# Kernel optimization log

Hardware: AMD Instinct MI355X
Metric: run time of the kernel (lower is better)

## Reference

```python
import jax, jax.numpy as jnp
import numpy as np

B, L, C = 4, 2048, 1024
H = 16
D = C // H  # head_dim = 64


def _rope(t, cos, sin):
    # t: [B, H, L, D]; cos/sin: [L, D//2] broadcast to [1, 1, L, D//2]
    te = t[..., ::2]
    to = t[..., 1::2]
    c = cos[None, None]
    s = sin[None, None]
    re = te * c - to * s
    ro = te * s + to * c
    # interleave even/odd back: [..., D//2, 2] -> [..., D]
    return jnp.stack([re, ro], axis=-1).reshape(t.shape)


def setup_inputs() -> dict:
    key = jax.random.key(0)
    ks = jax.random.split(key, 5)
    x = jax.random.normal(ks[0], (B, L, C), dtype=jnp.float32)
    # rotary phases: theta_i = 10000^(-2i/D), angles = pos * theta
    inv_freq = 1.0 / (10000.0 ** (np.arange(0, D, 2, dtype=np.float32) / D))
    ang = np.arange(L, dtype=np.float32)[:, None] * inv_freq[None, :]  # [L, D//2]
    cos = jnp.asarray(np.cos(ang))
    sin = jnp.asarray(np.sin(ang))
    w_qkv = jax.random.normal(ks[1], (3 * C, C), dtype=jnp.float32) * (C ** -0.5)
    w_proj = jax.random.normal(ks[2], (C, C), dtype=jnp.float32) * (C ** -0.5)
    b_proj = jnp.zeros((C,), dtype=jnp.float32)
    return {"x": x, "cos": cos, "sin": sin, "w_qkv": w_qkv, "w_proj": w_proj, "b_proj": b_proj}


def reference(x, cos, sin, w_qkv, w_proj, b_proj):
    Bx, Lx, Cx = x.shape
    # QKV projection (torch Linear: y = x @ W.T), then split heads
    qkv = jnp.einsum("blc,fc->blf", x, w_qkv)  # [B, L, 3C]
    qkv = qkv.reshape(Bx, Lx, 3, H, D).transpose(2, 0, 3, 1, 4)  # [3, B, H, L, D]
    q, k, v = qkv[0], qkv[1], qkv[2]
    q = _rope(q, cos, sin)
    k = _rope(k, cos, sin)
    # scaled dot-product attention, non-causal
    scale = D ** -0.5
    scores = jnp.einsum("bhqd,bhkd->bhqk", q, k) * scale
    attn = jax.nn.softmax(scores, axis=-1)
    o = jnp.einsum("bhqk,bhkd->bhqd", attn, v)  # [B, H, L, D]
    o = o.transpose(0, 2, 1, 3).reshape(Bx, Lx, Cx)
    return jnp.einsum("blc,fc->blf", o, w_proj) + b_proj
```

## Files before the change

kernel.cpp:

```cpp
#include <hip/hip_runtime.h>
#include <hip/hip_bf16.h>
#include <cstdint>


typedef unsigned short u16;
typedef __attribute__((ext_vector_type(8))) short bf16x8;
typedef __attribute__((ext_vector_type(4))) float f32x4;

#define GLD16(g, l)                                                            \
  __builtin_amdgcn_global_load_lds(                                            \
      (const __attribute__((address_space(1))) void*)(g),                      \
      (__attribute__((address_space(3))) void*)(l), 16, 0, 0)

static __device__ __forceinline__ u16 f32_bf16(float f) {
  union { float f; unsigned u; } v; v.f = f;
  unsigned r = v.u + 0x7FFFu + ((v.u >> 16) & 1u);
  return (u16)(r >> 16);
}
static __device__ __forceinline__ float bf16_f32(u16 h) {
  union { unsigned u; float f; } v; v.u = ((unsigned)h) << 16;
  return v.f;
}
static __device__ __forceinline__ unsigned pack_rne(float a, float b) {
  union { float f; unsigned u; } x, y; x.f = a; y.f = b;
  unsigned ua = x.u + 0x7FFFu + ((x.u >> 16) & 1u);
  unsigned ub = y.u + 0x7FFFu + ((y.u >> 16) & 1u);
  return (ua >> 16) | (ub & 0xFFFF0000u);
}
static __device__ __forceinline__ unsigned pack_bf16_hw(float a, float b) {
  float2 t; t.x = a; t.y = b;
  __hip_bfloat162 h = __float22bfloat162_rn(t);
  union { __hip_bfloat162 h; unsigned u; } c; c.h = h;
  return c.u;
}

__global__ __launch_bounds__(256) void convert_all(
    const void* __restrict__ x, const void* __restrict__ wq,
    const void* __restrict__ wp, const void* __restrict__ cs,
    const void* __restrict__ sn, const void* __restrict__ bs,
    u16* __restrict__ xb, u16* __restrict__ wqb, u16* __restrict__ wpb,
    u16* __restrict__ cb, u16* __restrict__ sb, u16* __restrict__ bb) {
  const unsigned f32mode = (((const unsigned*)cs)[0] == 0x3F800000u);
  int blk = blockIdx.x;
  const void* src; u16* dst; int i0, n4;
  if (blk < 8192)       { src = x;  dst = xb;  i0 = blk;         n4 = 2097152; }
  else if (blk < 11264) { src = wq; dst = wqb; i0 = blk - 8192;  n4 = 786432; }
  else if (blk < 12288) { src = wp; dst = wpb; i0 = blk - 11264; n4 = 262144; }
  else if (blk < 12352) { src = cs; dst = cb;  i0 = blk - 12288; n4 = 16384; }
  else if (blk < 12416) { src = sn; dst = sb;  i0 = blk - 12352; n4 = 16384; }
  else                  { src = bs; dst = bb;  i0 = blk - 12416; n4 = 256; }
  int i = i0 * 256 + threadIdx.x;
  if (i >= n4) return;
  if (f32mode) {
    float4 v = ((const float4*)src)[i];
    uint2 o;
    o.x = pack_rne(v.x, v.y);
    o.y = pack_rne(v.z, v.w);
    ((uint2*)dst)[i] = o;
  } else {
    ((uint2*)dst)[i] = ((const uint2*)src)[i];
  }
}

static __device__ __forceinline__ void gemm_mainloop(
    const u16* __restrict__ A, const u16* __restrict__ Bm, int K,
    int m0, int n0, u16* As, u16* Bs, f32x4 acc[4][4]) {
  const int tid  = threadIdx.x;
  const int lane = tid & 63;
  const int wave = tid >> 6;
  const int n16  = lane & 15;
  const int quad = lane >> 4;
  const int wm = (wave >> 1) * 64;
  const int wn = (wave & 1) * 64;
  const u16* ag = A  + (size_t)(m0 + wave * 16 + (lane >> 2)) * K + (lane & 3) * 8;
  const u16* bg = Bm + (size_t)(n0 + wave * 16 + (lane >> 2)) * K + (lane & 3) * 8;
  u16* al = As + wave * (16 * 32);
  u16* bl = Bs + wave * (16 * 32);
  for (int kt = 0; kt < K; kt += 32) {
    GLD16(ag + kt, al);
    GLD16(ag + (size_t)64 * K + kt, al + 64 * 32);
    GLD16(bg + kt, bl);
    GLD16(bg + (size_t)64 * K + kt, bl + 64 * 32);
    __syncthreads();
    bf16x8 af[4], bf[4];
#pragma unroll
    for (int i = 0; i < 4; i++)
      af[i] = *(const bf16x8*)(As + (wm + i * 16 + n16) * 32 + quad * 8);
#pragma unroll
    for (int j = 0; j < 4; j++)
      bf[j] = *(const bf16x8*)(Bs + (wn + j * 16 + n16) * 32 + quad * 8);
#pragma unroll
    for (int i = 0; i < 4; i++)
#pragma unroll
      for (int j = 0; j < 4; j++)
        acc[i][j] = __builtin_amdgcn_mfma_f32_16x16x32_bf16(af[i], bf[j], acc[i][j], 0, 0, 0);
    __syncthreads();
  }
}

__global__ __launch_bounds__(256) void gemm_qkv(
    const u16* __restrict__ x, const u16* __restrict__ w,
    u16* __restrict__ q_ws, u16* __restrict__ k_ws, u16* __restrict__ vt_ws) {
  __shared__ u16 As[128 * 32];
  __shared__ u16 Bs[128 * 32];
  f32x4 acc[4][4];
#pragma unroll
  for (int i = 0; i < 4; i++)
#pragma unroll
    for (int j = 0; j < 4; j++) acc[i][j] = (f32x4){0.f, 0.f, 0.f, 0.f};
  const int m0 = blockIdx.y * 128;
  const int n0 = blockIdx.x * 128;
  gemm_mainloop(x, w, 1024, m0, n0, As, Bs, acc);
  const int lane = threadIdx.x & 63, wave = threadIdx.x >> 6;
  const int n16 = lane & 15, quad = lane >> 4;
  const int wm = (wave >> 1) * 64, wn = (wave & 1) * 64;
#pragma unroll
  for (int i = 0; i < 4; i++)
#pragma unroll
    for (int j = 0; j < 4; j++) {
      int f = n0 + wn + j * 16 + n16;
      int which = f >> 10;
      int rem = f & 1023;
      int h = rem >> 6, d = rem & 63;
      int l0 = m0 + wm + i * 16 + quad * 4;
      int b = l0 >> 11, l = l0 & 2047;
      if (which == 2) {
        uint2 o;
        o.x = pack_rne(acc[i][j][0], acc[i][j][1]);
        o.y = pack_rne(acc[i][j][2], acc[i][j][3]);
        size_t idx = (((size_t)b * 16 + h) * 64 + d) * 2048 + l;
        *(uint2*)(vt_ws + idx) = o;
      } else {
        u16* dst = (which == 0) ? q_ws : k_ws;
        size_t base = (((size_t)b * 16 + h) * 2048 + l) * 64 + d;
#pragma unroll
        for (int r = 0; r < 4; r++)
          dst[base + (size_t)r * 64] = f32_bf16(acc[i][j][r]);
      }
    }
}

#define NP_ROPE 4194304
__global__ __launch_bounds__(256) void rope_qk(
    u16* __restrict__ q, u16* __restrict__ k,
    const u16* __restrict__ cosp, const u16* __restrict__ sinp) {
  int idx = blockIdx.x * 256 + threadIdx.x;
  bool isq = (idx < NP_ROPE);
  u16* t = isq ? q : k;
  float sc = isq ? 0.18033688011112042f : 1.0f;
  int p = isq ? idx : idx - NP_ROPE;
  int l = (p >> 5) & 2047;
  int i = p & 31;
  unsigned v = ((unsigned*)t)[p];
  float te = bf16_f32((u16)(v & 0xFFFFu));
  float to = bf16_f32((u16)(v >> 16));
  float c = bf16_f32(cosp[l * 32 + i]);
  float s = bf16_f32(sinp[l * 32 + i]);
  ((unsigned*)t)[p] = pack_rne((te * c - to * s) * sc, (te * s + to * c) * sc);
}

__global__ __launch_bounds__(256, 2) void flash_attn(
    const u16* __restrict__ q_ws, const u16* __restrict__ k_ws,
    const u16* __restrict__ vt_ws, u16* __restrict__ o_ws) {
  __shared__ u16 Ks[2][64 * 64];
  __shared__ u16 Vs[2][64 * 64];
  __shared__ u16 Pa[4 * 64 * 72];
  const int bh = blockIdx.x & 63;
  const int q0 = (blockIdx.x >> 6) * 256;
  const int b = bh >> 4, h = bh & 15;
  const int tid = threadIdx.x, lane = tid & 63, wave = tid >> 6;
  const int n16 = lane & 15, quad = lane >> 4;
  const int x7 = n16 & 7;
  const size_t hoff = (size_t)bh * (2048 * 64);

  bf16x8 qf[4][2];
#pragma unroll
  for (int qb = 0; qb < 4; qb++) {
    const u16* qrow = q_ws + hoff + (size_t)(q0 + wave * 64 + qb * 16 + n16) * 64;
    qf[qb][0] = *(const bf16x8*)(qrow + quad * 8);
    qf[qb][1] = *(const bf16x8*)(qrow + 32 + quad * 8);
  }

  f32x4 oacc[4][4];
  f32x4 lq[4];
#pragma unroll
  for (int qb = 0; qb < 4; qb++) {
    lq[qb] = (f32x4){0.f, 0.f, 0.f, 0.f};
#pragma unroll
    for (int s = 0; s < 4; s++) oacc[qb][s] = (f32x4){0.f, 0.f, 0.f, 0.f};
  }

  const int srow = wave * 8 + (lane >> 3);
  const int sw = (lane & 7) ^ ((lane >> 3) & 7);
  const u16* kg = k_ws + hoff + (size_t)srow * 64 + sw * 8;
  const u16* vg = vt_ws + hoff + (size_t)srow * 2048 + sw * 8;
  const int loff = wave * 8 * 64;
  u16* const pw = Pa + wave * (64 * 72);

  GLD16(kg, &Ks[0][loff]);
  GLD16(kg + 32 * 64, &Ks[0][loff + 32 * 64]);
  GLD16(vg, &Vs[0][loff]);
  GLD16(vg + (size_t)32 * 2048, &Vs[0][loff + 32 * 64]);

  for (int kt = 0; kt < 2048; kt += 64) {
    const int buf = (kt >> 6) & 1;
    __syncthreads();
    if (kt + 64 < 2048) {
      const u16* kgn = kg + (size_t)(kt + 64) * 64;
      const u16* vgn = vg + (kt + 64);
      GLD16(kgn, &Ks[buf ^ 1][loff]);
      GLD16(kgn + 32 * 64, &Ks[buf ^ 1][loff + 32 * 64]);
      GLD16(vgn, &Vs[buf ^ 1][loff]);
      GLD16(vgn + (size_t)32 * 2048, &Vs[buf ^ 1][loff + 32 * 64]);
    }
    const u16* ks = Ks[buf];
    const u16* vs = Vs[buf];

#pragma unroll
    for (int sub = 0; sub < 4; sub++) {
      const u16* krow = ks + (sub * 16 + n16) * 64;
      bf16x8 kf0 = *(const bf16x8*)(krow + (quad ^ x7) * 8);
      bf16x8 kf1 = *(const bf16x8*)(krow + ((quad + 4) ^ x7) * 8);
#pragma unroll
      for (int qb = 0; qb < 4; qb++) {
        f32x4 z = (f32x4){0.f, 0.f, 0.f, 0.f};
        z = __builtin_amdgcn_mfma_f32_16x16x32_bf16(kf0, qf[qb][0], z, 0, 0, 0);
        z = __builtin_amdgcn_mfma_f32_16x16x32_bf16(kf1, qf[qb][1], z, 0, 0, 0);
        f32x4 p;
#pragma unroll
        for (int r = 0; r < 4; r++) p[r] = __builtin_amdgcn_exp2f(z[r]);
        lq[qb] += p;
        uint2 o;
        o.x = pack_bf16_hw(p[0], p[1]);
        o.y = pack_bf16_hw(p[2], p[3]);
        *(uint2*)(pw + (qb * 16 + n16) * 72 + quad * 4 + sub * 16) = o;
      }
    }

    bf16x8 pf[4][2];
#pragma unroll
    for (int qb = 0; qb < 4; qb++) {
      const u16* prow = pw + (qb * 16 + n16) * 72;
      pf[qb][0] = *(const bf16x8*)(prow + quad * 8);
      pf[qb][1] = *(const bf16x8*)(prow + 32 + quad * 8);
    }
#pragma unroll
    for (int sd = 0; sd < 4; sd++) {
      const u16* vrow = vs + (sd * 16 + n16) * 64;
      bf16x8 vf0 = *(const bf16x8*)(vrow + (quad ^ x7) * 8);
      bf16x8 vf1 = *(const bf16x8*)(vrow + ((quad + 4) ^ x7) * 8);
#pragma unroll
      for (int qb = 0; qb < 4; qb++) {
        oacc[qb][sd] = __builtin_amdgcn_mfma_f32_16x16x32_bf16(pf[qb][0], vf0, oacc[qb][sd], 0, 0, 0);
        oacc[qb][sd] = __builtin_amdgcn_mfma_f32_16x16x32_bf16(pf[qb][1], vf1, oacc[qb][sd], 0, 0, 0);
      }
    }
  }

#pragma unroll
  for (int qb = 0; qb < 4; qb++) {
    float l = lq[qb][0] + lq[qb][1] + lq[qb][2] + lq[qb][3];
    l += __shfl_xor(l, 16, 64);
    l += __shfl_xor(l, 32, 64);
    float linv = 1.0f / l;
#pragma unroll
    for (int r = 0; r < 4; r++) {
      float lr = __shfl(linv, quad * 4 + r, 64);
      int row = q0 + wave * 64 + qb * 16 + quad * 4 + r;
      size_t base = ((size_t)b * 2048 + row) * 1024 + h * 64;
#pragma unroll
      for (int sd = 0; sd < 4; sd++)
        o_ws[base + sd * 16 + n16] = f32_bf16(oacc[qb][sd][r] * lr);
    }
  }
}

__global__ __launch_bounds__(256) void gemm_proj(
    const u16* __restrict__ o, const u16* __restrict__ w,
    const u16* __restrict__ bias, float* __restrict__ out) {
  __shared__ u16 As[128 * 32];
  __shared__ u16 Bs[128 * 32];
  f32x4 acc[4][4];
#pragma unroll
  for (int i = 0; i < 4; i++)
#pragma unroll
    for (int j = 0; j < 4; j++) acc[i][j] = (f32x4){0.f, 0.f, 0.f, 0.f};
  const int m0 = blockIdx.y * 128;
  const int n0 = blockIdx.x * 128;
  gemm_mainloop(o, w, 1024, m0, n0, As, Bs, acc);
  const int lane = threadIdx.x & 63, wave = threadIdx.x >> 6;
  const int n16 = lane & 15, quad = lane >> 4;
  const int wm = (wave >> 1) * 64, wn = (wave & 1) * 64;
#pragma unroll
  for (int i = 0; i < 4; i++)
#pragma unroll
    for (int j = 0; j < 4; j++) {
      int f = n0 + wn + j * 16 + n16;
      float bf = bf16_f32(bias[f]);
#pragma unroll
      for (int r = 0; r < 4; r++) {
        int m = m0 + wm + i * 16 + quad * 4 + r;
        out[(size_t)m * 1024 + f] = acc[i][j][r] + bf;
      }
    }
}

extern "C" void kernel_launch(void* const* d_in, const int* in_sizes, int n_in,
                              void* d_out, int out_size, void* d_ws, size_t ws_size,
                              hipStream_t stream) {
  float* out = (float*)d_out;

  u16* ws = (u16*)d_ws;
  u16* xb     = ws;
  u16* wqkvb  = ws + 8388608;
  u16* wprojb = ws + 11534336;
  u16* cosb   = ws + 12582912;
  u16* sinb   = ws + 12648448;
  u16* biasb  = ws + 12713984;
  u16* qb     = ws + 12715008;
  u16* kb     = ws + 21103616;
  u16* vtb    = ws + 29492224;
  u16* ob     = xb;

  convert_all<<<12417, 256, 0, stream>>>(
      d_in[0], d_in[3], d_in[4], d_in[1], d_in[2], d_in[5],
      xb, wqkvb, wprojb, cosb, sinb, biasb);

  gemm_qkv<<<dim3(24, 64), 256, 0, stream>>>(xb, wqkvb, qb, kb, vtb);
  rope_qk<<<32768, 256, 0, stream>>>(qb, kb, cosb, sinb);
  flash_attn<<<512, 256, 0, stream>>>(qb, kb, vtb, ob);
  gemm_proj<<<dim3(8, 64), 256, 0, stream>>>(ob, wprojb, biasb, out);
}
```

Measured before the change: 286.5 us.

## Fuse RoPE and Q scaling into QKV GEMM epilogue via swapped MFMA operands

Removes the separate rope_qk kernel and applies rotary embedding and the query scale directly in the QKV GEMM epilogue for Q and K tiles. Q/K blocks swap the MFMA A/B operands so each lane holds four consecutive head-dim values, letting it rotate even/odd pairs in registers and write packed 8-byte stores. This avoids a full read-modify-write pass over Q and K in global memory and one kernel launch. RoPE now operates on fp32 accumulators before bf16 rounding, and the epilogue reads cos/sin tables per tile.

```diff
diff --git a/kernel.cpp b/kernel.cpp
--- a/kernel.cpp
+++ b/kernel.cpp
@@ -62,6 +62,7 @@
   }
 }
 
+template <bool SWAP>
 static __device__ __forceinline__ void gemm_mainloop(
     const u16* __restrict__ A, const u16* __restrict__ Bm, int K,
     int m0, int n0, u16* As, u16* Bs, f32x4 acc[4][4]) {
@@ -93,13 +94,16 @@
     for (int i = 0; i < 4; i++)
 #pragma unroll
       for (int j = 0; j < 4; j++)
-        acc[i][j] = __builtin_amdgcn_mfma_f32_16x16x32_bf16(af[i], bf[j], acc[i][j], 0, 0, 0);
+        acc[i][j] = SWAP
+            ? __builtin_amdgcn_mfma_f32_16x16x32_bf16(bf[j], af[i], acc[i][j], 0, 0, 0)
+            : __builtin_amdgcn_mfma_f32_16x16x32_bf16(af[i], bf[j], acc[i][j], 0, 0, 0);
     __syncthreads();
   }
 }
 
 __global__ __launch_bounds__(256) void gemm_qkv(
     const u16* __restrict__ x, const u16* __restrict__ w,
+    const u16* __restrict__ cosb, const u16* __restrict__ sinb,
     u16* __restrict__ q_ws, u16* __restrict__ k_ws, u16* __restrict__ vt_ws) {
   __shared__ u16 As[128 * 32];
   __shared__ u16 Bs[128 * 32];
@@ -110,53 +114,55 @@
     for (int j = 0; j < 4; j++) acc[i][j] = (f32x4){0.f, 0.f, 0.f, 0.f};
   const int m0 = blockIdx.y * 128;
   const int n0 = blockIdx.x * 128;
-  gemm_mainloop(x, w, 1024, m0, n0, As, Bs, acc);
   const int lane = threadIdx.x & 63, wave = threadIdx.x >> 6;
   const int n16 = lane & 15, quad = lane >> 4;
   const int wm = (wave >> 1) * 64, wn = (wave & 1) * 64;
-#pragma unroll
-  for (int i = 0; i < 4; i++)
-#pragma unroll
-    for (int j = 0; j < 4; j++) {
-      int f = n0 + wn + j * 16 + n16;
-      int which = f >> 10;
-      int rem = f & 1023;
-      int h = rem >> 6, d = rem & 63;
-      int l0 = m0 + wm + i * 16 + quad * 4;
-      int b = l0 >> 11, l = l0 & 2047;
-      if (which == 2) {
+
+  if (blockIdx.x < 16) {
+    gemm_mainloop<true>(x, w, 1024, m0, n0, As, Bs, acc);
+    const bool isq = (blockIdx.x < 8);
+    const float sc = isq ? 0.18033688011112042f : 1.0f;
+    u16* const dst = isq ? q_ws : k_ws;
+#pragma unroll
+    for (int i = 0; i < 4; i++) {
+      int lg = m0 + wm + i * 16 + n16;
+      int b = lg >> 11, l = lg & 2047;
+#pragma unroll
+      for (int j = 0; j < 4; j++) {
+        int fl = (n0 & 1023) + wn + j * 16 + quad * 4;
+        int h = fl >> 6;
+        int d0 = fl & 63;
+        int i0 = d0 >> 1;
+        unsigned cw = *(const unsigned*)(cosb + l * 32 + i0);
+        unsigned sw = *(const unsigned*)(sinb + l * 32 + i0);
+        float c0 = bf16_f32((u16)(cw & 0xFFFFu)), c1 = bf16_f32((u16)(cw >> 16));
+        float s0 = bf16_f32((u16)(sw & 0xFFFFu)), s1 = bf16_f32((u16)(sw >> 16));
+        float te0 = acc[i][j][0], to0 = acc[i][j][1];
+        float te1 = acc[i][j][2], to1 = acc[i][j][3];
+        uint2 o;
+        o.x = pack_rne((te0 * c0 - to0 * s0) * sc, (te0 * s0 + to0 * c0) * sc);
+        o.y = pack_rne((te1 * c1 - to1 * s1) * sc, (te1 * s1 + to1 * c1) * sc);
+        *(uint2*)(dst + (((size_t)b * 16 + h) * 2048 + l) * 64 + d0) = o;
+      }
+    }
+  } else {
+    gemm_mainloop<false>(x, w, 1024, m0, n0, As, Bs, acc);
+#pragma unroll
+    for (int i = 0; i < 4; i++)
+#pragma unroll
+      for (int j = 0; j < 4; j++) {
+        int f = n0 + wn + j * 16 + n16;
+        int rem = f & 1023;
+        int h = rem >> 6, d = rem & 63;
+        int l0 = m0 + wm + i * 16 + quad * 4;
+        int b = l0 >> 11, l = l0 & 2047;
         uint2 o;
         o.x = pack_rne(acc[i][j][0], acc[i][j][1]);
         o.y = pack_rne(acc[i][j][2], acc[i][j][3]);
         size_t idx = (((size_t)b * 16 + h) * 64 + d) * 2048 + l;
         *(uint2*)(vt_ws + idx) = o;
-      } else {
-        u16* dst = (which == 0) ? q_ws : k_ws;
-        size_t base = (((size_t)b * 16 + h) * 2048 + l) * 64 + d;
-#pragma unroll
-        for (int r = 0; r < 4; r++)
-          dst[base + (size_t)r * 64] = f32_bf16(acc[i][j][r]);
-      }
-    }
-}
-
-#define NP_ROPE 4194304
-__global__ __launch_bounds__(256) void rope_qk(
-    u16* __restrict__ q, u16* __restrict__ k,
-    const u16* __restrict__ cosp, const u16* __restrict__ sinp) {
-  int idx = blockIdx.x * 256 + threadIdx.x;
-  bool isq = (idx < NP_ROPE);
-  u16* t = isq ? q : k;
-  float sc = isq ? 0.18033688011112042f : 1.0f;
-  int p = isq ? idx : idx - NP_ROPE;
-  int l = (p >> 5) & 2047;
-  int i = p & 31;
-  unsigned v = ((unsigned*)t)[p];
-  float te = bf16_f32((u16)(v & 0xFFFFu));
-  float to = bf16_f32((u16)(v >> 16));
-  float c = bf16_f32(cosp[l * 32 + i]);
-  float s = bf16_f32(sinp[l * 32 + i]);
-  ((unsigned*)t)[p] = pack_rne((te * c - to * s) * sc, (te * s + to * c) * sc);
+      }
+  }
 }
 
 __global__ __launch_bounds__(256, 2) void flash_attn(
@@ -287,7 +293,7 @@
     for (int j = 0; j < 4; j++) acc[i][j] = (f32x4){0.f, 0.f, 0.f, 0.f};
   const int m0 = blockIdx.y * 128;
   const int n0 = blockIdx.x * 128;
-  gemm_mainloop(o, w, 1024, m0, n0, As, Bs, acc);
+  gemm_mainloop<false>(o, w, 1024, m0, n0, As, Bs, acc);
   const int lane = threadIdx.x & 63, wave = threadIdx.x >> 6;
   const int n16 = lane & 15, quad = lane >> 4;
   const int wm = (wave >> 1) * 64, wn = (wave & 1) * 64;
@@ -326,8 +332,7 @@
       d_in[0], d_in[3], d_in[4], d_in[1], d_in[2], d_in[5],
       xb, wqkvb, wprojb, cosb, sinb, biasb);
 
-  gemm_qkv<<<dim3(24, 64), 256, 0, stream>>>(xb, wqkvb, qb, kb, vtb);
-  rope_qk<<<32768, 256, 0, stream>>>(qb, kb, cosb, sinb);
+  gemm_qkv<<<dim3(24, 64), 256, 0, stream>>>(xb, wqkvb, cosb, sinb, qb, kb, vtb);
   flash_attn<<<512, 256, 0, stream>>>(qb, kb, vtb, ob);
   gemm_proj<<<dim3(8, 64), 256, 0, stream>>>(ob, wprojb, biasb, out);
 }
```

After: 287.1 us. Within noise of the previous version (+0.2%).
